# Performance work log

Hardware: AMD Instinct MI355X
Metric: run time of the kernel (lower is better)

The kernel has to match this reference:

```python
import jax, jax.numpy as jnp
import numpy as np

N_NODES = 100000
N_EDGES = 1600000
FEAT = 128
HID = 128
CLASSES = 10
GRAPHS = 64


def gcn_conv(x, W, b, src, dst, n):
    # PyG GCNConv: h = x @ W; add self-loops; symmetric deg^{-1/2} norm; scatter-add; + bias
    h = x @ W
    src_f = jnp.concatenate([src, jnp.arange(n, dtype=src.dtype)])
    dst_f = jnp.concatenate([dst, jnp.arange(n, dtype=dst.dtype)])
    deg = jax.ops.segment_sum(jnp.ones_like(dst_f, dtype=h.dtype), dst_f, num_segments=n)
    dinv = jax.lax.rsqrt(jnp.where(deg > 0, deg, 1.0))
    norm = dinv[src_f] * dinv[dst_f]              # [E+N]
    msg = h[src_f] * norm[:, None]                # gather + scale
    out = jax.ops.segment_sum(msg, dst_f, num_segments=n)  # scatter-add
    return out + b


def global_mean_pool(x, batch, num_graphs):
    s = jax.ops.segment_sum(x, batch, num_segments=num_graphs)
    cnt = jax.ops.segment_sum(jnp.ones_like(batch, dtype=x.dtype), batch, num_segments=num_graphs)
    return s / jnp.maximum(cnt, 1.0)[:, None]


def setup_inputs() -> dict:
    key = jax.random.key(0)
    ks = jax.random.split(key, 10)
    x = jax.random.normal(ks[0], (N_NODES, FEAT), dtype=jnp.float32)
    edge_index = jax.random.randint(ks[1], (2, N_EDGES), 0, N_NODES, dtype=jnp.int64)
    batch = jnp.sort(jax.random.randint(ks[2], (N_NODES,), 0, GRAPHS, dtype=jnp.int64))
    def glorot(k, fi, fo):
        s = float(np.sqrt(6.0 / (fi + fo)))
        return jax.random.uniform(k, (fi, fo), jnp.float32, -s, s)
    return {
        "x": x, "edge_index": edge_index, "batch": batch,
        "W1": glorot(ks[3], FEAT, HID), "b1": jnp.zeros((HID,), jnp.float32),
        "W2": glorot(ks[4], HID, HID), "b2": jnp.zeros((HID,), jnp.float32),
        "W3": glorot(ks[5], HID, HID), "b3": jnp.zeros((HID,), jnp.float32),
        "Wlin": glorot(ks[6], HID, CLASSES), "blin": jnp.zeros((CLASSES,), jnp.float32),
    }


def reference(x, edge_index, batch, W1, b1, W2, b2, W3, b3, Wlin, blin):
    src, dst = edge_index[0], edge_index[1]
    n = x.shape[0]
    h = jax.nn.relu(gcn_conv(x, W1, b1, src, dst, n))
    h = jax.nn.relu(gcn_conv(h, W2, b2, src, dst, n))
    h = gcn_conv(h, W3, b3, src, dst, n)
    emb = global_mean_pool(h, batch, GRAPHS)      # [GRAPHS, HID]
    # dropout(p=0.5) is identity in eval mode
    logits = emb @ Wlin + blin                    # [GRAPHS, CLASSES]
    return logits, jnp.squeeze(emb)
```

## Files before the change

### kernel.cpp

```cpp
#include <hip/hip_runtime.h>
#include <hip/hip_bf16.h>
#include <stdint.h>

typedef unsigned int uint32;
typedef __attribute__((ext_vector_type(8))) short short8;
typedef __attribute__((ext_vector_type(4))) float float4v;

#define FEAT 128
#define NGRAPH 64
#define GB   256
#define NBK  512

__device__ __forceinline__ float bf2f_lo(uint32 v) {
    union { uint32 i; float f; } u; u.i = v << 16; return u.f;
}
__device__ __forceinline__ float bf2f_hi(uint32 v) {
    union { uint32 i; float f; } u; u.i = v & 0xffff0000u; return u.f;
}
__device__ __forceinline__ unsigned short f2bf(float f) {
    uint32 u = __builtin_bit_cast(uint32, f);
    uint32 r = (u + 0x7fffu + ((u >> 16) & 1u)) >> 16;
    return (unsigned short)r;
}
__device__ __forceinline__ uint32 f2bf2(float lo, float hi) {
    return (uint32)f2bf(lo) | ((uint32)f2bf(hi) << 16);
}

__global__ void k_bhist(const int* __restrict__ dst, int* __restrict__ bhistT,
                        float* __restrict__ pool, int* __restrict__ cntg,
                        const float* __restrict__ W1, const float* __restrict__ W2,
                        const float* __restrict__ W3, unsigned short* __restrict__ o1,
                        unsigned short* __restrict__ o2, unsigned short* __restrict__ o3,
                        int E) {
    int t = threadIdx.x, blk = blockIdx.x;
    if (blk >= GB) {
        int b2 = blk - GB;
        int wid = b2 >> 3;
        const float* W = (wid == 0) ? W1 : (wid == 1) ? W2 : W3;
        unsigned short* out = (wid == 0) ? o1 : (wid == 1) ? o2 : o3;
        int e = (b2 & 7) * 256 + t;
        int kt = e >> 9, ct = (e >> 6) & 7, lane = e & 63;
        int krow = kt * 32 + (lane >> 4) * 8;
        int col = ct * 16 + (lane & 15);
#pragma unroll
        for (int j = 0; j < 8; j++)
            out[e * 8 + j] = f2bf(W[(krow + j) * FEAT + col]);
        return;
    }
    __shared__ int h[NBK];
    if (blk == 0) {
        for (int i = t; i < NGRAPH * FEAT; i += 256) pool[i] = 0.f;
        if (t < NGRAPH) cntg[t] = 0;
    }
    for (int b = t; b < NBK; b += 256) h[b] = 0;
    __syncthreads();
    int chunk = (E + GB - 1) / GB;
    int lo = blk * chunk, hi = min(lo + chunk, E);
    for (int e = lo + t; e < hi; e += 256)
        atomicAdd(&h[dst[e] >> 8], 1);
    __syncthreads();
    for (int b = t; b < NBK; b += 256) bhistT[b * GB + blk] = h[b];
}

__global__ void k_boffs_a(int* __restrict__ bhistT, int* __restrict__ btot) {
    int b = blockIdx.x, l = threadIdx.x;
    int v[4];
    int base = b * GB + l * 4;
#pragma unroll
    for (int j = 0; j < 4; j++) v[j] = bhistT[base + j];
    int s = v[0] + v[1] + v[2] + v[3];
    int incl = s;
    for (int off = 1; off < 64; off <<= 1) {
        int u = __shfl_up(incl, off);
        if (l >= off) incl += u;
    }
    int excl = incl - s;
    int p0 = excl, p1 = p0 + v[0], p2 = p1 + v[1], p3 = p2 + v[2];
    bhistT[base + 0] = p0; bhistT[base + 1] = p1;
    bhistT[base + 2] = p2; bhistT[base + 3] = p3;
    if (l == 63) btot[b] = incl;
}

__global__ void k_boffs_b(const int* __restrict__ btot, int* __restrict__ bbase) {
    __shared__ int sc[NBK];
    int t = threadIdx.x;
    int s = btot[t];
    sc[t] = s;
    __syncthreads();
    for (int off = 1; off < NBK; off <<= 1) {
        int v = (t >= off) ? sc[t - off] : 0;
        __syncthreads();
        sc[t] += v;
        __syncthreads();
    }
    bbase[t] = sc[t] - s;
    if (t == NBK - 1) bbase[NBK] = sc[t];
}

__global__ void k_bscat(const int* __restrict__ src, const int* __restrict__ dst,
                        const int* __restrict__ bhistT, const int* __restrict__ bbase,
                        uint32* __restrict__ ebuf, int E) {
    __shared__ int cur[NBK];
    int t = threadIdx.x, blk = blockIdx.x;
    for (int b = t; b < NBK; b += 256) cur[b] = bbase[b] + bhistT[b * GB + blk];
    __syncthreads();
    int chunk = (E + GB - 1) / GB;
    int lo = blk * chunk, hi = min(lo + chunk, E);
    for (int e = lo + t; e < hi; e += 256) {
        int d = dst[e], s = src[e];
        int b = d >> 8;
        int p = atomicAdd(&cur[b], 1);
        ebuf[p] = ((uint32)s << 8) | (uint32)(d & 255);
    }
}

__global__ void k_csr(const uint32* __restrict__ ebuf, const int* __restrict__ bbase,
                      float* __restrict__ dinv, int* __restrict__ rowp,
                      int* __restrict__ csrc, int N, int E) {
    __shared__ int h[256];
    __shared__ int cur[256];
    int t = threadIdx.x, b = blockIdx.x;
    h[t] = 0;
    __syncthreads();
    int e0 = bbase[b], e1 = bbase[b + 1];
    for (int e = e0 + t; e < e1; e += 256)
        atomicAdd(&h[ebuf[e] & 255u], 1);
    __syncthreads();
    int deg = h[t];
    cur[t] = deg;
    __syncthreads();
    for (int off = 1; off < 256; off <<= 1) {
        int v = (t >= off) ? cur[t - off] : 0;
        __syncthreads();
        cur[t] += v;
        __syncthreads();
    }
    int r = bbase[b] + cur[t] - deg;
    int node = b * 256 + t;
    if (node < N) {
        rowp[node] = r;
        dinv[node] = rsqrtf((float)deg + 1.0f);
    }
    if (b == 0 && t == 0) rowp[N] = E;
    cur[t] = r;
    __syncthreads();
    for (int e = e0 + t; e < e1; e += 256) {
        uint32 v = ebuf[e];
        int p = atomicAdd(&cur[v & 255u], 1);
        csrc[p] = (int)(v >> 8);
    }
}

template <bool F32IN>
__global__ void k_gemm(const void* __restrict__ Xp,
                       const unsigned short* __restrict__ Wswz,
                       const float* __restrict__ dinv,
                       unsigned short* __restrict__ Hb, int N) {
    __shared__ unsigned short Wl[FEAT * FEAT];
    {
        const uint4* Wg = (const uint4*)Wswz;
        uint4* Ws = (uint4*)Wl;
        for (int i = threadIdx.x; i < 2048; i += 256) Ws[i] = Wg[i];
    }
    __syncthreads();

    int wave = threadIdx.x >> 6, lane = threadIdx.x & 63;
    int r0 = (blockIdx.x * 4 + wave) * 16;
    if (r0 >= N) return;
    int m = lane & 15, q = lane >> 4;

    int arow = r0 + m; if (arow >= N) arow = N - 1;
    short8 a[4];
    if (F32IN) {
        const float* Ar = (const float*)Xp + (long)arow * FEAT;
#pragma unroll
        for (int kt = 0; kt < 4; kt++) {
            float4 u = *(const float4*)(Ar + kt * 32 + q * 8);
            float4 v = *(const float4*)(Ar + kt * 32 + q * 8 + 4);
            short8 tv;
            tv[0] = (short)f2bf(u.x); tv[1] = (short)f2bf(u.y);
            tv[2] = (short)f2bf(u.z); tv[3] = (short)f2bf(u.w);
            tv[4] = (short)f2bf(v.x); tv[5] = (short)f2bf(v.y);
            tv[6] = (short)f2bf(v.z); tv[7] = (short)f2bf(v.w);
            a[kt] = tv;
        }
    } else {
        const short8* Ar = (const short8*)((const unsigned short*)Xp + (long)arow * FEAT);
#pragma unroll
        for (int kt = 0; kt < 4; kt++) a[kt] = Ar[kt * 4 + q];
    }

    const short8* Bl = (const short8*)Wl;
    float4v acc[8];
#pragma unroll
    for (int ct = 0; ct < 8; ct++) acc[ct] = (float4v){0.f, 0.f, 0.f, 0.f};
#pragma unroll
    for (int ct = 0; ct < 8; ct++) {
        acc[ct] = __builtin_amdgcn_mfma_f32_16x16x32_bf16(Bl[(0 * 8 + ct) * 64 + lane], a[0], acc[ct], 0, 0, 0);
        acc[ct] = __builtin_amdgcn_mfma_f32_16x16x32_bf16(Bl[(1 * 8 + ct) * 64 + lane], a[1], acc[ct], 0, 0, 0);
        acc[ct] = __builtin_amdgcn_mfma_f32_16x16x32_bf16(Bl[(2 * 8 + ct) * 64 + lane], a[2], acc[ct], 0, 0, 0);
        acc[ct] = __builtin_amdgcn_mfma_f32_16x16x32_bf16(Bl[(3 * 8 + ct) * 64 + lane], a[3], acc[ct], 0, 0, 0);
    }

    int node = r0 + m;
    bool ok = (node < N);
    float d = ok ? dinv[node] : 0.f;
#pragma unroll
    for (int ct = 0; ct < 8; ct++) {
        if (ok) {
            uint2 o;
            o.x = f2bf2(acc[ct][0] * d, acc[ct][1] * d);
            o.y = f2bf2(acc[ct][2] * d, acc[ct][3] * d);
            ((uint2*)(Hb + (long)node * FEAT + ct * 16))[q] = o;
        }
    }
}

__global__ void k_agg(const uint32* __restrict__ Hb,
                      const int* __restrict__ rowp, const int* __restrict__ csrc,
                      const float* __restrict__ dinv, const float* __restrict__ bias,
                      uint32* __restrict__ OUTb, int N, int relu) {
    int wave = threadIdx.x >> 6, lane = threadIdx.x & 63;
    int i = blockIdx.x * 4 + wave;
    if (i >= N) return;
    int f = lane & 15, quarter = lane >> 4;
    const uint4* H4 = (const uint4*)Hb;
    float a0 = 0.f, a1 = 0.f, a2 = 0.f, a3 = 0.f;
    float a4 = 0.f, a5 = 0.f, a6 = 0.f, a7 = 0.f;
    int e0 = rowp[i], e1 = rowp[i + 1];
    int e = e0;
    for (; e + 16 <= e1; e += 16) {
        int  s[4];
        uint4 h[4];
#pragma unroll
        for (int j = 0; j < 4; j++) s[j] = csrc[e + 4 * j + quarter];
#pragma unroll
        for (int j = 0; j < 4; j++) h[j] = H4[(long)s[j] * 16 + f];
#pragma unroll
        for (int j = 0; j < 4; j++) {
            a0 += bf2f_lo(h[j].x); a1 += bf2f_hi(h[j].x);
            a2 += bf2f_lo(h[j].y); a3 += bf2f_hi(h[j].y);
            a4 += bf2f_lo(h[j].z); a5 += bf2f_hi(h[j].z);
            a6 += bf2f_lo(h[j].w); a7 += bf2f_hi(h[j].w);
        }
    }
    {
        int r = e1 - e;
        int  s[4];
        uint4 h[4];
#pragma unroll
        for (int j = 0; j < 4; j++) {
            int idx = 4 * j + quarter;
            if (idx < r) s[j] = csrc[e + idx];
        }
#pragma unroll
        for (int j = 0; j < 4; j++)
            if (4 * j + quarter < r) h[j] = H4[(long)s[j] * 16 + f];
#pragma unroll
        for (int j = 0; j < 4; j++)
            if (4 * j + quarter < r) {
                a0 += bf2f_lo(h[j].x); a1 += bf2f_hi(h[j].x);
                a2 += bf2f_lo(h[j].y); a3 += bf2f_hi(h[j].y);
                a4 += bf2f_lo(h[j].z); a5 += bf2f_hi(h[j].z);
                a6 += bf2f_lo(h[j].w); a7 += bf2f_hi(h[j].w);
            }
    }
    a0 += __shfl_xor(a0, 16); a1 += __shfl_xor(a1, 16);
    a2 += __shfl_xor(a2, 16); a3 += __shfl_xor(a3, 16);
    a4 += __shfl_xor(a4, 16); a5 += __shfl_xor(a5, 16);
    a6 += __shfl_xor(a6, 16); a7 += __shfl_xor(a7, 16);
    a0 += __shfl_xor(a0, 32); a1 += __shfl_xor(a1, 32);
    a2 += __shfl_xor(a2, 32); a3 += __shfl_xor(a3, 32);
    a4 += __shfl_xor(a4, 32); a5 += __shfl_xor(a5, 32);
    a6 += __shfl_xor(a6, 32); a7 += __shfl_xor(a7, 32);
    if (quarter == 0) {
        uint4 hv = H4[(long)i * 16 + f];
        a0 += bf2f_lo(hv.x); a1 += bf2f_hi(hv.x);
        a2 += bf2f_lo(hv.y); a3 += bf2f_hi(hv.y);
        a4 += bf2f_lo(hv.z); a5 += bf2f_hi(hv.z);
        a6 += bf2f_lo(hv.w); a7 += bf2f_hi(hv.w);
        float di = dinv[i];
        const float4* b4 = (const float4*)bias;
        float4 bb0 = b4[2 * f], bb1 = b4[2 * f + 1];
        a0 = a0 * di + bb0.x; a1 = a1 * di + bb0.y;
        a2 = a2 * di + bb0.z; a3 = a3 * di + bb0.w;
        a4 = a4 * di + bb1.x; a5 = a5 * di + bb1.y;
        a6 = a6 * di + bb1.z; a7 = a7 * di + bb1.w;
        if (relu) {
            a0 = fmaxf(a0, 0.f); a1 = fmaxf(a1, 0.f);
            a2 = fmaxf(a2, 0.f); a3 = fmaxf(a3, 0.f);
            a4 = fmaxf(a4, 0.f); a5 = fmaxf(a5, 0.f);
            a6 = fmaxf(a6, 0.f); a7 = fmaxf(a7, 0.f);
        }
        uint4 o;
        o.x = f2bf2(a0, a1);
        o.y = f2bf2(a2, a3);
        o.z = f2bf2(a4, a5);
        o.w = f2bf2(a6, a7);
        ((uint4*)OUTb)[(long)i * 16 + f] = o;
    }
}

__global__ void k_pool(const uint32* __restrict__ Gb, const int* __restrict__ batch,
                       float* __restrict__ pool, int* __restrict__ cntg, int N) {
    int t = threadIdx.x;
    int nb = gridDim.x;
    int chunk = (N + nb - 1) / nb;
    int lo = blockIdx.x * chunk, hi = min(lo + chunk, N);
    if (lo >= hi) return;
    float ax = 0.f, ay = 0.f;
    int cnt = 0;
    int cg = batch[lo];
    for (int i = lo; i < hi; i++) {
        int g = batch[i];
        if (g != cg) {
            atomicAdd(&pool[cg * FEAT + 2 * t], ax);
            atomicAdd(&pool[cg * FEAT + 2 * t + 1], ay);
            if (t == 0) atomicAdd(&cntg[cg], cnt);
            ax = ay = 0.f; cnt = 0; cg = g;
        }
        uint32 v = Gb[(long)i * 64 + t];
        ax += bf2f_lo(v); ay += bf2f_hi(v);
        cnt++;
    }
    atomicAdd(&pool[cg * FEAT + 2 * t], ax);
    atomicAdd(&pool[cg * FEAT + 2 * t + 1], ay);
    if (t == 0) atomicAdd(&cntg[cg], cnt);
}

__global__ void k_final(const float* __restrict__ pool, const int* __restrict__ cntg,
                        const float* __restrict__ Wlin, const float* __restrict__ blin,
                        float* __restrict__ out) {
    __shared__ float es[FEAT];
    int g = blockIdx.x, t = threadIdx.x;
    float c = (float)max(cntg[g], 1);
    float e = pool[g * FEAT + t] / c;
    es[t] = e;
    out[NGRAPH * 10 + g * FEAT + t] = e;
    __syncthreads();
    if (t < 10) {
        float a = blin[t];
        for (int k = 0; k < FEAT; k++)
            a += es[k] * Wlin[k * 10 + t];
        out[g * 10 + t] = a;
    }
}

extern "C" void kernel_launch(void* const* d_in, const int* in_sizes, int n_in,
                              void* d_out, int out_size, void* d_ws, size_t ws_size,
                              hipStream_t stream) {
    const float* x    = (const float*)d_in[0];
    const int*   ei   = (const int*)d_in[1];
    const int*   batch= (const int*)d_in[2];
    const float* W1   = (const float*)d_in[3];
    const float* b1   = (const float*)d_in[4];
    const float* W2   = (const float*)d_in[5];
    const float* b2   = (const float*)d_in[6];
    const float* W3   = (const float*)d_in[7];
    const float* b3   = (const float*)d_in[8];
    const float* Wlin = (const float*)d_in[9];
    const float* blin = (const float*)d_in[10];

    const int N = in_sizes[2];
    const int E = in_sizes[1] / 2;
    const int* src = ei;
    const int* dst = ei + E;
    const int NB = (N + 255) >> 8;

    char* w = (char*)d_ws;
    auto take = [&](size_t bytes) {
        char* p = w;
        w += (bytes + 255) & ~(size_t)255;
        return p;
    };
    float*  dinv   = (float*) take((size_t)N * 4);
    int*    rowp   = (int*)   take((size_t)(N + 1) * 4);
    int*    csrc   = (int*)   take((size_t)E * 4);
    uint32* ebuf   = (uint32*)take((size_t)E * 4);
    int*    bhistT = (int*)   take((size_t)GB * NBK * 4);
    int*    btot   = (int*)   take((size_t)NBK * 4);
    int*    bbase  = (int*)   take((size_t)(NBK + 1) * 4);
    uint32* hbuf   = (uint32*)take((size_t)N * FEAT * 2);
    uint32* gbuf   = (uint32*)take((size_t)N * FEAT * 2);
    unsigned short* w1s = (unsigned short*)take(FEAT * FEAT * 2);
    unsigned short* w2s = (unsigned short*)take(FEAT * FEAT * 2);
    unsigned short* w3s = (unsigned short*)take(FEAT * FEAT * 2);
    float*  pool   = (float*) take((size_t)NGRAPH * FEAT * 4);
    int*    cntg   = (int*)   take((size_t)NGRAPH * 4);
    (void)ws_size; (void)n_in; (void)out_size;

    k_bhist  <<<GB + 24, 256, 0, stream>>>(dst, bhistT, pool, cntg,
                                           W1, W2, W3, w1s, w2s, w3s, E);
    k_boffs_a<<<NBK, 64, 0, stream>>>(bhistT, btot);
    k_boffs_b<<<1, NBK, 0, stream>>>(btot, bbase);
    k_bscat  <<<GB, 256, 0, stream>>>(src, dst, bhistT, bbase, ebuf, E);
    k_csr    <<<NB, 256, 0, stream>>>(ebuf, bbase, dinv, rowp, csrc, N, E);

    const int tile_blocks = (N + 63) / 64;
    const int agg_blocks  = (N + 3) / 4;

    k_gemm<true> <<<tile_blocks, 256, 0, stream>>>(x, w1s, dinv, (unsigned short*)hbuf, N);
    k_agg<<<agg_blocks, 256, 0, stream>>>(hbuf, rowp, csrc, dinv, b1, gbuf, N, 1);
    k_gemm<false><<<tile_blocks, 256, 0, stream>>>(gbuf, w2s, dinv, (unsigned short*)hbuf, N);
    k_agg<<<agg_blocks, 256, 0, stream>>>(hbuf, rowp, csrc, dinv, b2, gbuf, N, 1);
    k_gemm<false><<<tile_blocks, 256, 0, stream>>>(gbuf, w3s, dinv, (unsigned short*)hbuf, N);
    k_agg<<<agg_blocks, 256, 0, stream>>>(hbuf, rowp, csrc, dinv, b3, gbuf, N, 0);

    k_pool <<<4096, 64, 0, stream>>>(gbuf, batch, pool, cntg, N);
    k_final<<<NGRAPH, 128, 0, stream>>>(pool, cntg, Wlin, blin, (float*)d_out);
}
```

Baseline: 412.1 us.

## Fuse global mean pooling into final aggregation kernel and pack accumulators as float2

The last aggregation layer now adds its per-node results straight into per-graph pool sums, via two shared-memory slots per block followed by global atomics. This removes both the bf16 write of the final node features and the separate pooling kernel's reread of them. RELU and POOL become template parameters, and the accumulators are packed into float2 vectors so the compiler can emit packed adds. The cost is extra shared atomics, block barriers in the last layer, and the assumption that each 4-node block spans at most two graphs, which relies on batch being sorted.

```diff
diff --git a/kernel.cpp b/kernel.cpp
--- a/kernel.cpp
+++ b/kernel.cpp
@@ -5,6 +5,7 @@
 typedef unsigned int uint32;
 typedef __attribute__((ext_vector_type(8))) short short8;
 typedef __attribute__((ext_vector_type(4))) float float4v;
+typedef __attribute__((ext_vector_type(2))) float f32x2;
 
 #define FEAT 128
 #define NGRAPH 64
@@ -216,116 +217,131 @@
     }
 }
 
+template <int RELU, int POOL>
 __global__ void k_agg(const uint32* __restrict__ Hb,
                       const int* __restrict__ rowp, const int* __restrict__ csrc,
                       const float* __restrict__ dinv, const float* __restrict__ bias,
-                      uint32* __restrict__ OUTb, int N, int relu) {
+                      uint32* __restrict__ OUTb, const int* __restrict__ batch,
+                      float* __restrict__ pool, int* __restrict__ cntg, int N) {
+    __shared__ float sp[2][FEAT];
+    __shared__ int scnt[2];
     int wave = threadIdx.x >> 6, lane = threadIdx.x & 63;
     int i = blockIdx.x * 4 + wave;
-    if (i >= N) return;
+    if (POOL) {
+        for (int k = threadIdx.x; k < 2 * FEAT; k += 256) (&sp[0][0])[k] = 0.f;
+        if (threadIdx.x < 2) scnt[threadIdx.x] = 0;
+        __syncthreads();
+    } else {
+        if (i >= N) return;
+    }
+    bool active = (i < N);
     int f = lane & 15, quarter = lane >> 4;
     const uint4* H4 = (const uint4*)Hb;
-    float a0 = 0.f, a1 = 0.f, a2 = 0.f, a3 = 0.f;
-    float a4 = 0.f, a5 = 0.f, a6 = 0.f, a7 = 0.f;
-    int e0 = rowp[i], e1 = rowp[i + 1];
-    int e = e0;
-    for (; e + 16 <= e1; e += 16) {
-        int  s[4];
-        uint4 h[4];
-#pragma unroll
-        for (int j = 0; j < 4; j++) s[j] = csrc[e + 4 * j + quarter];
-#pragma unroll
-        for (int j = 0; j < 4; j++) h[j] = H4[(long)s[j] * 16 + f];
-#pragma unroll
-        for (int j = 0; j < 4; j++) {
-            a0 += bf2f_lo(h[j].x); a1 += bf2f_hi(h[j].x);
-            a2 += bf2f_lo(h[j].y); a3 += bf2f_hi(h[j].y);
-            a4 += bf2f_lo(h[j].z); a5 += bf2f_hi(h[j].z);
-            a6 += bf2f_lo(h[j].w); a7 += bf2f_hi(h[j].w);
-        }
-    }
-    {
-        int r = e1 - e;
-        int  s[4];
-        uint4 h[4];
-#pragma unroll
-        for (int j = 0; j < 4; j++) {
-            int idx = 4 * j + quarter;
-            if (idx < r) s[j] = csrc[e + idx];
-        }
-#pragma unroll
-        for (int j = 0; j < 4; j++)
-            if (4 * j + quarter < r) h[j] = H4[(long)s[j] * 16 + f];
-#pragma unroll
-        for (int j = 0; j < 4; j++)
-            if (4 * j + quarter < r) {
-                a0 += bf2f_lo(h[j].x); a1 += bf2f_hi(h[j].x);
-                a2 += bf2f_lo(h[j].y); a3 += bf2f_hi(h[j].y);
-                a4 += bf2f_lo(h[j].z); a5 += bf2f_hi(h[j].z);
-                a6 += bf2f_lo(h[j].w); a7 += bf2f_hi(h[j].w);
+    f32x2 c0 = {0.f, 0.f}, c1 = c0, c2 = c0, c3 = c0;
+    if (active) {
+        int e0 = rowp[i], e1 = rowp[i + 1];
+        int e = e0;
+        for (; e + 16 <= e1; e += 16) {
+            int  s[4];
+            uint4 h[4];
+#pragma unroll
+            for (int j = 0; j < 4; j++) s[j] = csrc[e + 4 * j + quarter];
+#pragma unroll
+            for (int j = 0; j < 4; j++) h[j] = H4[(long)s[j] * 16 + f];
+#pragma unroll
+            for (int j = 0; j < 4; j++) {
+                f32x2 u;
+                u.x = bf2f_lo(h[j].x); u.y = bf2f_hi(h[j].x); c0 += u;
+                u.x = bf2f_lo(h[j].y); u.y = bf2f_hi(h[j].y); c1 += u;
+                u.x = bf2f_lo(h[j].z); u.y = bf2f_hi(h[j].z); c2 += u;
+                u.x = bf2f_lo(h[j].w); u.y = bf2f_hi(h[j].w); c3 += u;
             }
-    }
-    a0 += __shfl_xor(a0, 16); a1 += __shfl_xor(a1, 16);
-    a2 += __shfl_xor(a2, 16); a3 += __shfl_xor(a3, 16);
-    a4 += __shfl_xor(a4, 16); a5 += __shfl_xor(a5, 16);
-    a6 += __shfl_xor(a6, 16); a7 += __shfl_xor(a7, 16);
-    a0 += __shfl_xor(a0, 32); a1 += __shfl_xor(a1, 32);
-    a2 += __shfl_xor(a2, 32); a3 += __shfl_xor(a3, 32);
-    a4 += __shfl_xor(a4, 32); a5 += __shfl_xor(a5, 32);
-    a6 += __shfl_xor(a6, 32); a7 += __shfl_xor(a7, 32);
-    if (quarter == 0) {
-        uint4 hv = H4[(long)i * 16 + f];
-        a0 += bf2f_lo(hv.x); a1 += bf2f_hi(hv.x);
-        a2 += bf2f_lo(hv.y); a3 += bf2f_hi(hv.y);
-        a4 += bf2f_lo(hv.z); a5 += bf2f_hi(hv.z);
-        a6 += bf2f_lo(hv.w); a7 += bf2f_hi(hv.w);
-        float di = dinv[i];
-        const float4* b4 = (const float4*)bias;
-        float4 bb0 = b4[2 * f], bb1 = b4[2 * f + 1];
-        a0 = a0 * di + bb0.x; a1 = a1 * di + bb0.y;
-        a2 = a2 * di + bb0.z; a3 = a3 * di + bb0.w;
-        a4 = a4 * di + bb1.x; a5 = a5 * di + bb1.y;
-        a6 = a6 * di + bb1.z; a7 = a7 * di + bb1.w;
-        if (relu) {
-            a0 = fmaxf(a0, 0.f); a1 = fmaxf(a1, 0.f);
-            a2 = fmaxf(a2, 0.f); a3 = fmaxf(a3, 0.f);
-            a4 = fmaxf(a4, 0.f); a5 = fmaxf(a5, 0.f);
-            a6 = fmaxf(a6, 0.f); a7 = fmaxf(a7, 0.f);
-        }
-        uint4 o;
-        o.x = f2bf2(a0, a1);
-        o.y = f2bf2(a2, a3);
-        o.z = f2bf2(a4, a5);
-        o.w = f2bf2(a6, a7);
-        ((uint4*)OUTb)[(long)i * 16 + f] = o;
-    }
-}
-
-__global__ void k_pool(const uint32* __restrict__ Gb, const int* __restrict__ batch,
-                       float* __restrict__ pool, int* __restrict__ cntg, int N) {
-    int t = threadIdx.x;
-    int nb = gridDim.x;
-    int chunk = (N + nb - 1) / nb;
-    int lo = blockIdx.x * chunk, hi = min(lo + chunk, N);
-    if (lo >= hi) return;
-    float ax = 0.f, ay = 0.f;
-    int cnt = 0;
-    int cg = batch[lo];
-    for (int i = lo; i < hi; i++) {
-        int g = batch[i];
-        if (g != cg) {
-            atomicAdd(&pool[cg * FEAT + 2 * t], ax);
-            atomicAdd(&pool[cg * FEAT + 2 * t + 1], ay);
-            if (t == 0) atomicAdd(&cntg[cg], cnt);
-            ax = ay = 0.f; cnt = 0; cg = g;
-        }
-        uint32 v = Gb[(long)i * 64 + t];
-        ax += bf2f_lo(v); ay += bf2f_hi(v);
-        cnt++;
-    }
-    atomicAdd(&pool[cg * FEAT + 2 * t], ax);
-    atomicAdd(&pool[cg * FEAT + 2 * t + 1], ay);
-    if (t == 0) atomicAdd(&cntg[cg], cnt);
+        }
+        {
+            int r = e1 - e;
+            int  s[4];
+            uint4 h[4];
+#pragma unroll
+            for (int j = 0; j < 4; j++) {
+                int idx = 4 * j + quarter;
+                if (idx < r) s[j] = csrc[e + idx];
+            }
+#pragma unroll
+            for (int j = 0; j < 4; j++)
+                if (4 * j + quarter < r) h[j] = H4[(long)s[j] * 16 + f];
+#pragma unroll
+            for (int j = 0; j < 4; j++)
+                if (4 * j + quarter < r) {
+                    f32x2 u;
+                    u.x = bf2f_lo(h[j].x); u.y = bf2f_hi(h[j].x); c0 += u;
+                    u.x = bf2f_lo(h[j].y); u.y = bf2f_hi(h[j].y); c1 += u;
+                    u.x = bf2f_lo(h[j].z); u.y = bf2f_hi(h[j].z); c2 += u;
+                    u.x = bf2f_lo(h[j].w); u.y = bf2f_hi(h[j].w); c3 += u;
+                }
+        }
+        c0.x += __shfl_xor(c0.x, 16); c0.y += __shfl_xor(c0.y, 16);
+        c1.x += __shfl_xor(c1.x, 16); c1.y += __shfl_xor(c1.y, 16);
+        c2.x += __shfl_xor(c2.x, 16); c2.y += __shfl_xor(c2.y, 16);
+        c3.x += __shfl_xor(c3.x, 16); c3.y += __shfl_xor(c3.y, 16);
+        c0.x += __shfl_xor(c0.x, 32); c0.y += __shfl_xor(c0.y, 32);
+        c1.x += __shfl_xor(c1.x, 32); c1.y += __shfl_xor(c1.y, 32);
+        c2.x += __shfl_xor(c2.x, 32); c2.y += __shfl_xor(c2.y, 32);
+        c3.x += __shfl_xor(c3.x, 32); c3.y += __shfl_xor(c3.y, 32);
+        if (quarter == 0) {
+            uint4 hv = H4[(long)i * 16 + f];
+            c0.x += bf2f_lo(hv.x); c0.y += bf2f_hi(hv.x);
+            c1.x += bf2f_lo(hv.y); c1.y += bf2f_hi(hv.y);
+            c2.x += bf2f_lo(hv.z); c2.y += bf2f_hi(hv.z);
+            c3.x += bf2f_lo(hv.w); c3.y += bf2f_hi(hv.w);
+            float di = dinv[i];
+            const float4* b4 = (const float4*)bias;
+            float4 bb0 = b4[2 * f], bb1 = b4[2 * f + 1];
+            c0.x = c0.x * di + bb0.x; c0.y = c0.y * di + bb0.y;
+            c1.x = c1.x * di + bb0.z; c1.y = c1.y * di + bb0.w;
+            c2.x = c2.x * di + bb1.x; c2.y = c2.y * di + bb1.y;
+            c3.x = c3.x * di + bb1.z; c3.y = c3.y * di + bb1.w;
+            if (RELU) {
+                c0.x = fmaxf(c0.x, 0.f); c0.y = fmaxf(c0.y, 0.f);
+                c1.x = fmaxf(c1.x, 0.f); c1.y = fmaxf(c1.y, 0.f);
+                c2.x = fmaxf(c2.x, 0.f); c2.y = fmaxf(c2.y, 0.f);
+                c3.x = fmaxf(c3.x, 0.f); c3.y = fmaxf(c3.y, 0.f);
+            }
+            if (!POOL) {
+                uint4 o;
+                o.x = f2bf2(c0.x, c0.y);
+                o.y = f2bf2(c1.x, c1.y);
+                o.z = f2bf2(c2.x, c2.y);
+                o.w = f2bf2(c3.x, c3.y);
+                ((uint4*)OUTb)[(long)i * 16 + f] = o;
+            } else {
+                int gi = batch[i];
+                int g0 = batch[blockIdx.x * 4];
+                int slot = (gi == g0) ? 0 : 1;
+                float* sd = sp[slot] + f * 8;
+                atomicAdd(&sd[0], c0.x); atomicAdd(&sd[1], c0.y);
+                atomicAdd(&sd[2], c1.x); atomicAdd(&sd[3], c1.y);
+                atomicAdd(&sd[4], c2.x); atomicAdd(&sd[5], c2.y);
+                atomicAdd(&sd[6], c3.x); atomicAdd(&sd[7], c3.y);
+                if (f == 0) atomicAdd(&scnt[slot], 1);
+            }
+        }
+    }
+    if (POOL) {
+        __syncthreads();
+        int i0 = blockIdx.x * 4;
+        if (i0 < N) {
+            int t = threadIdx.x;
+            int g0 = batch[i0];
+            int g1 = batch[min(i0 + 3, N - 1)];
+            if (t < FEAT) {
+                atomicAdd(&pool[g0 * FEAT + t], sp[0][t]);
+            } else if (t < 2 * FEAT && g1 != g0) {
+                atomicAdd(&pool[g1 * FEAT + (t - FEAT)], sp[1][t - FEAT]);
+            }
+            if (t == 0) atomicAdd(&cntg[g0], scnt[0]);
+            if (t == 1 && g1 != g0) atomicAdd(&cntg[g1], scnt[1]);
+        }
+    }
 }
 
 __global__ void k_final(const float* __restrict__ pool, const int* __restrict__ cntg,
@@ -400,12 +416,14 @@
     const int agg_blocks  = (N + 3) / 4;
 
     k_gemm<true> <<<tile_blocks, 256, 0, stream>>>(x, w1s, dinv, (unsigned short*)hbuf, N);
-    k_agg<<<agg_blocks, 256, 0, stream>>>(hbuf, rowp, csrc, dinv, b1, gbuf, N, 1);
+    k_agg<1, 0><<<agg_blocks, 256, 0, stream>>>(hbuf, rowp, csrc, dinv, b1, gbuf,
+                                                batch, pool, cntg, N);
     k_gemm<false><<<tile_blocks, 256, 0, stream>>>(gbuf, w2s, dinv, (unsigned short*)hbuf, N);
-    k_agg<<<agg_blocks, 256, 0, stream>>>(hbuf, rowp, csrc, dinv, b2, gbuf, N, 1);
+    k_agg<1, 0><<<agg_blocks, 256, 0, stream>>>(hbuf, rowp, csrc, dinv, b2, gbuf,
+                                                batch, pool, cntg, N);
     k_gemm<false><<<tile_blocks, 256, 0, stream>>>(gbuf, w3s, dinv, (unsigned short*)hbuf, N);
-    k_agg<<<agg_blocks, 256, 0, stream>>>(hbuf, rowp, csrc, dinv, b3, gbuf, N, 0);
-
-    k_pool <<<4096, 64, 0, stream>>>(gbuf, batch, pool, cntg, N);
+    k_agg<0, 1><<<agg_blocks, 256, 0, stream>>>(hbuf, rowp, csrc, dinv, b3, gbuf,
+                                                batch, pool, cntg, N);
+
     k_final<<<NGRAPH, 128, 0, stream>>>(pool, cntg, Wlin, blin, (float*)d_out);
 }
```

Result: slower. 570.4 us (+38.4%).
